# Performance work log

Hardware: AMD Instinct MI355X
Metric: run time of the kernel (lower is better)

## Reference

```python
import jax, jax.numpy as jnp
import numpy as np
from math import sqrt

DIM = 256
HEADS = 4
GROUPS = min(DIM // 4, 32)  # = 32
EPS = 1e-6


def setup_inputs() -> dict:
    key = jax.random.key(0)
    ks = jax.random.split(key, 10)
    B, C, H, W = 16, DIM, 32, 32
    x = jax.random.normal(ks[0], (B, C, H, W), dtype=jnp.float32)
    s = 1.0 / sqrt(C)
    inp = {
        'x': x,
        'gn_scale': jnp.ones((C,), jnp.float32),
        'gn_bias': jnp.zeros((C,), jnp.float32),
        'Wq': jax.random.normal(ks[1], (C, C), jnp.float32) * s,
        'bq': jnp.zeros((C,), jnp.float32),
        'Wk': jax.random.normal(ks[2], (C, C), jnp.float32) * s,
        'bk': jnp.zeros((C,), jnp.float32),
        'Wv': jax.random.normal(ks[3], (C, C), jnp.float32) * s,
        'bv': jnp.zeros((C,), jnp.float32),
        'Wp': jax.random.normal(ks[4], (C, C), jnp.float32) * s,
        'bp': jnp.zeros((C,), jnp.float32),
    }
    return inp


def _group_norm(x, scale, bias):
    B, C, H, W = x.shape
    xg = x.reshape(B, GROUPS, C // GROUPS, H, W)
    mean = xg.mean(axis=(2, 3, 4), keepdims=True)
    var = xg.var(axis=(2, 3, 4), keepdims=True)
    xg = (xg - mean) * jax.lax.rsqrt(var + EPS)
    x = xg.reshape(B, C, H, W)
    return x * scale[None, :, None, None] + bias[None, :, None, None]


def _lin_ch(x, W, b):
    # 1x1 conv / linear over channel dim: (B,C,H,W) x (C,Cout) -> (B,Cout,H,W)
    return jnp.einsum('bchw,cd->bdhw', x, W) + b[None, :, None, None]


def reference(x, gn_scale, gn_bias, Wq, bq, Wk, bk, Wv, bv, Wp, bp):
    B, C, H, W = x.shape
    dh = C // HEADS
    _x = _group_norm(x, gn_scale, gn_bias)
    q = _lin_ch(_x, Wq, bq).reshape(B, HEADS, dh, H, W)
    k = _lin_ch(_x, Wk, bk).reshape(B, HEADS, dh, H, W)
    v = _lin_ch(_x, Wv, bv).reshape(B, HEADS, dh, H, W)
    scores = jnp.einsum('bhdxy,bhdij->bhxyij', q, k) / sqrt(C)
    scores = scores.reshape(B, HEADS, H, W, H * W)
    weights = jax.nn.softmax(scores, axis=-1).reshape(B, HEADS, H, W, H, W)
    h = jnp.einsum('bhxyij,bhdij->bhdxy', weights, v).reshape(B, C, H, W)
    h = _lin_ch(h, Wp, bp)
    ret = (x + h) / sqrt(2.0)
    return ret
```

## Files before the change

kernel.cpp:

```cpp
#include <hip/hip_runtime.h>
#include <hip/hip_bf16.h>

#define BATCH 16
#define CH    256
#define HW    1024
#define NH    4
#define DH    64
#define NG    32
#define CPG   8
#define EPSV  1e-6f

#define QSCALE 0.090168440055558706f

typedef __bf16 bf16x8 __attribute__((ext_vector_type(8)));
typedef float  f32x4  __attribute__((ext_vector_type(4)));

__device__ __forceinline__ unsigned short f2bf(float f) {
    union { __hip_bfloat16 h; unsigned short u; } cv;
    cv.h = __float2bfloat16(f);
    return cv.u;
}

__device__ __forceinline__ unsigned int fbits(float f) {
    union { float f; unsigned int u; } cv; cv.f = f; return cv.u;
}

__device__ __forceinline__ void gld_lds16(const unsigned short* g, unsigned short* l) {
    __builtin_amdgcn_global_load_lds(
        (const __attribute__((address_space(1))) void*)g,
        (__attribute__((address_space(3))) void*)l, 16, 0, 0);
}

__global__ void prep_kernel(const float* Wq, const float* Wk, const float* Wv,
                            const float* Wp, const float* bq, const float* bk,
                            const float* bv, unsigned short* wqkv_t,
                            unsigned short* wp_t, float* bqkv) {
    int idx = blockIdx.x * 256 + threadIdx.x;
    if (idx < 768 * 256) {
        int n = idx >> 8, c = idx & 255;
        const float* W = (n < 256) ? Wq : (n < 512) ? Wk : Wv;
        int d = n & 255;
        wqkv_t[idx] = f2bf(W[c * 256 + d]);
    } else if (idx < 768 * 256 + 256 * 256) {
        int j = idx - 768 * 256;
        int n = j >> 8, c = j & 255;
        wp_t[j] = f2bf(Wp[c * 256 + n]);
    }
    if (idx < 768)
        bqkv[idx] = (idx < 256) ? bq[idx] : (idx < 512) ? bk[idx - 256] : bv[idx - 512];
}

__global__ void gn_stats_kernel(const float* x, const float* scale, const float* bias,
                                float* coefA, float* coefB) {
    int bg = blockIdx.x;
    const float4* p = reinterpret_cast<const float4*>(x + (size_t)bg * (CPG * HW));
    int t = threadIdx.x;
    float s = 0.f, ss = 0.f;
    for (int i = t; i < CPG * HW / 4; i += 256) {
        float4 v = p[i];
        s += v.x + v.y + v.z + v.w;
        ss += v.x * v.x + v.y * v.y + v.z * v.z + v.w * v.w;
    }
    for (int o = 32; o; o >>= 1) { s += __shfl_down(s, o); ss += __shfl_down(ss, o); }
    __shared__ float as[4], ass[4];
    int w = t >> 6;
    if ((t & 63) == 0) { as[w] = s; ass[w] = ss; }
    __syncthreads();
    if (t < 8) {
        float S = as[0] + as[1] + as[2] + as[3];
        float SS = ass[0] + ass[1] + ass[2] + ass[3];
        float mean = S / (float)(CPG * HW);
        float var = SS / (float)(CPG * HW) - mean * mean;
        float rstd = rsqrtf(var + EPSV);
        int b = bg >> 5, g = bg & 31;
        int c = g * CPG + t;
        float a = rstd * scale[c];
        coefA[b * CH + c] = a;
        coefB[b * CH + c] = bias[c] - mean * a;
    }
}

__global__ __launch_bounds__(256) void qkv_kernel(const float* x,
        const float* coefA, const float* coefB,
        const unsigned short* wqkv_t, const float* bqkv,
        unsigned short* qb, unsigned short* kb, unsigned short* vb) {
    int t = threadIdx.x;
    int wv = t >> 6, lane = t & 63, quad = lane >> 4, ln = lane & 15;
    int wr = wv >> 1, wc = wv & 1;
    int bx = blockIdx.x;
    int m0 = bx * 128 + wr * 64;
    int n0 = blockIdx.y * 128 + wc * 64;
    int bb = bx >> 3;
    int p0 = (bx & 7) * 128;

    __shared__ __align__(16) unsigned short lds_a[128][40];

    const float* xb = x + (size_t)bb * CH * HW + p0;
    const float* cA = coefA + bb * CH;
    const float* cB = coefB + bb * CH;

    int sp = t & 127;
    int sbase = (t >> 7) * 2;

    f32x4 acc[4][4] = {};
    for (int k0 = 0; k0 < CH; k0 += 32) {
        bf16x8 wpk[2];
#pragma unroll
        for (int rep = 0; rep < 2; rep++) {
            int s = sbase + rep;
            int cb = k0 + s * 8;
            union { bf16x8 v8; __hip_bfloat162 h2[4]; } u;
#pragma unroll
            for (int j = 0; j < 4; j++) {
                float v0 = fmaf(xb[(size_t)(cb + 2 * j)     * HW + sp], cA[cb + 2 * j],     cB[cb + 2 * j]);
                float v1 = fmaf(xb[(size_t)(cb + 2 * j + 1) * HW + sp], cA[cb + 2 * j + 1], cB[cb + 2 * j + 1]);
                u.h2[j] = __float22bfloat162_rn(float2{v0, v1});
            }
            wpk[rep] = u.v8;
        }
        __syncthreads();
#pragma unroll
        for (int rep = 0; rep < 2; rep++) {
            int s = sbase + rep;
            int phys = s ^ (sp & 3);
            *reinterpret_cast<bf16x8*>(&lds_a[sp][phys * 8]) = wpk[rep];
        }
        __syncthreads();
        bf16x8 af[4], bfr[4];
#pragma unroll
        for (int i = 0; i < 4; i++) {
            int p = wr * 64 + i * 16 + ln;
            af[i] = *reinterpret_cast<const bf16x8*>(&lds_a[p][(quad ^ (p & 3)) * 8]);
        }
#pragma unroll
        for (int j = 0; j < 4; j++)
            bfr[j] = *reinterpret_cast<const bf16x8*>(
                wqkv_t + (size_t)(n0 + j * 16 + ln) * CH + k0 + quad * 8);
#pragma unroll
        for (int i = 0; i < 4; i++)
#pragma unroll
            for (int j = 0; j < 4; j++)
                acc[i][j] = __builtin_amdgcn_mfma_f32_16x16x32_bf16(af[i], bfr[j], acc[i][j], 0, 0, 0);
    }
#pragma unroll
    for (int j = 0; j < 4; j++) {
        int n = n0 + j * 16 + ln;
        float bias = bqkv[n];
        int which = n >> 8;
        int dh_ = n & 255;
        int head = dh_ >> 6, d = dh_ & 63;
#pragma unroll
        for (int i = 0; i < 4; i++) {
            int mb = m0 + i * 16 + quad * 4;
            int bi = mb >> 10, p = mb & 1023;
            int bh = bi * NH + head;
            if (which < 2) {
                unsigned short* dst = (which == 0 ? qb : kb) + (size_t)bh * HW * DH;
                float sc = (which == 0) ? QSCALE : 1.0f;
#pragma unroll
                for (int r = 0; r < 4; r++)
                    dst[(size_t)(p + r) * DH + d] = f2bf((acc[i][j][r] + bias) * sc);
            } else {
                unsigned short* dst = vb + ((size_t)bh * DH + d) * HW + p;
                ushort4 pk4;
                pk4.x = f2bf(acc[i][j][0] + bias);
                pk4.y = f2bf(acc[i][j][1] + bias);
                pk4.z = f2bf(acc[i][j][2] + bias);
                pk4.w = f2bf(acc[i][j][3] + bias);
                *reinterpret_cast<ushort4*>(dst) = pk4;
            }
        }
    }
}

__global__ __launch_bounds__(256) void attn_kernel(const unsigned short* qb,
        const unsigned short* kb, const unsigned short* vb, unsigned short* h_t) {
    int qblk = blockIdx.x, bh = blockIdx.y;
    int t = threadIdx.x;
    int wv = t >> 6, lane = t & 63, quad = lane >> 4, ln = lane & 15;
    int q0 = qblk * 128 + wv * 32;

    const unsigned short* Q = qb + (size_t)bh * HW * DH;
    const unsigned short* K = kb + (size_t)bh * HW * DH;
    const unsigned short* V = vb + (size_t)bh * DH * HW;

    __shared__ __align__(16) unsigned short kbuf[2][4096];
    __shared__ __align__(16) unsigned short vbuf[2][4096];
    __shared__ __align__(16) unsigned short pbuf[4][2][16][72];

    int c_a = wv * 64 + lane;
    int c_b = 256 + wv * 64 + lane;
    int pa = c_a >> 3, ja = (c_a & 7) ^ (pa & 7);
    int pb = c_b >> 3, jb = (c_b & 7) ^ (pb & 7);
    const unsigned short* pka = K + (size_t)pa * DH + ja * 8;
    const unsigned short* pkb = K + (size_t)pb * DH + jb * 8;
    const unsigned short* pva = V + (size_t)pa * HW + ja * 8;
    const unsigned short* pvb = V + (size_t)pb * HW + jb * 8;
    int lofs_a = wv * 512, lofs_b = 2048 + wv * 512;

    int koffs[4][2];
#pragma unroll
    for (int mt = 0; mt < 4; mt++) {
        int p = mt * 16 + ln, sw = p & 7;
#pragma unroll
        for (int kk = 0; kk < 2; kk++)
            koffs[mt][kk] = p * 64 + (((kk * 4 + quad) ^ sw) * 8);
    }

    bf16x8 qf[2][2];
#pragma unroll
    for (int nq = 0; nq < 2; nq++)
#pragma unroll
        for (int kk = 0; kk < 2; kk++)
            qf[nq][kk] = *reinterpret_cast<const bf16x8*>(
                Q + (size_t)(q0 + nq * 16 + ln) * DH + kk * 32 + quad * 8);

    f32x4 ls[2] = {};
    f32x4 o[2][4] = {};

    gld_lds16(pka, &kbuf[0][lofs_a]);
    gld_lds16(pkb, &kbuf[0][lofs_b]);
    gld_lds16(pva, &vbuf[0][lofs_a]);
    gld_lds16(pvb, &vbuf[0][lofs_b]);
    pka += 64 * DH; pkb += 64 * DH; pva += 64; pvb += 64;

#define ATTN_TILE(B, DO_STAGE)                                                      \
    {                                                                               \
        __syncthreads();                                                            \
        if (DO_STAGE) {                                                             \
            gld_lds16(pka, &kbuf[B ^ 1][lofs_a]);                                   \
            gld_lds16(pkb, &kbuf[B ^ 1][lofs_b]);                                   \
            gld_lds16(pva, &vbuf[B ^ 1][lofs_a]);                                   \
            gld_lds16(pvb, &vbuf[B ^ 1][lofs_b]);                                   \
            pka += 64 * DH; pkb += 64 * DH; pva += 64; pvb += 64;                   \
        }                                                                           \
        bf16x8 kf[4][2], vf[4][2];                                                  \
        _Pragma("unroll")                                                           \
        for (int mt = 0; mt < 4; mt++) {                                            \
            _Pragma("unroll")                                                       \
            for (int kk = 0; kk < 2; kk++) {                                        \
                kf[mt][kk] = *reinterpret_cast<const bf16x8*>(&kbuf[B][koffs[mt][kk]]); \
                vf[mt][kk] = *reinterpret_cast<const bf16x8*>(&vbuf[B][koffs[mt][kk]]); \
            }                                                                       \
        }                                                                           \
        f32x4 s[2][4] = {};                                                         \
        _Pragma("unroll")                                                           \
        for (int nq = 0; nq < 2; nq++)                                              \
            _Pragma("unroll")                                                       \
            for (int mt = 0; mt < 4; mt++) {                                        \
                s[nq][mt] = __builtin_amdgcn_mfma_f32_16x16x32_bf16(kf[mt][0], qf[nq][0], s[nq][mt], 0, 0, 0); \
                s[nq][mt] = __builtin_amdgcn_mfma_f32_16x16x32_bf16(kf[mt][1], qf[nq][1], s[nq][mt], 0, 0, 0); \
            }                                                                       \
        _Pragma("unroll")                                                           \
        for (int nq = 0; nq < 2; nq++)                                              \
            _Pragma("unroll")                                                       \
            for (int mt = 0; mt < 4; mt++) {                                        \
                float e0 = __builtin_amdgcn_exp2f(s[nq][mt][0]);                    \
                float e1 = __builtin_amdgcn_exp2f(s[nq][mt][1]);                    \
                float e2 = __builtin_amdgcn_exp2f(s[nq][mt][2]);                    \
                float e3 = __builtin_amdgcn_exp2f(s[nq][mt][3]);                    \
                ls[nq][0] += e0; ls[nq][1] += e1;                                   \
                ls[nq][2] += e2; ls[nq][3] += e3;                                   \
                uint2 pk2;                                                          \
                pk2.x = __builtin_amdgcn_perm(fbits(e1), fbits(e0), 0x07060302u);   \
                pk2.y = __builtin_amdgcn_perm(fbits(e3), fbits(e2), 0x07060302u);   \
                *reinterpret_cast<uint2*>(&pbuf[wv][nq][ln][mt * 16 + quad * 4]) = pk2; \
            }                                                                       \
        _Pragma("unroll")                                                           \
        for (int nq = 0; nq < 2; nq++)                                              \
            _Pragma("unroll")                                                       \
            for (int kk = 0; kk < 2; kk++) {                                        \
                bf16x8 pf = *reinterpret_cast<const bf16x8*>(&pbuf[wv][nq][ln][kk * 32 + quad * 8]); \
                _Pragma("unroll")                                                   \
                for (int mt = 0; mt < 4; mt++)                                      \
                    o[nq][mt] = __builtin_amdgcn_mfma_f32_16x16x32_bf16(vf[mt][kk], pf, o[nq][mt], 0, 0, 0); \
            }                                                                       \
    }

    for (int u = 0; u < 8; u++) {
        ATTN_TILE(0, true)
        ATTN_TILE(1, (u < 7))
    }
#undef ATTN_TILE

    int b_ = bh >> 2, head = bh & 3;
#pragma unroll
    for (int nq = 0; nq < 2; nq++) {
        float lsum = ls[nq][0] + ls[nq][1] + ls[nq][2] + ls[nq][3];
        lsum += __shfl_xor(lsum, 16);
        lsum += __shfl_xor(lsum, 32);
        float inv = 1.0f / lsum;
        unsigned short* dst = h_t + ((size_t)b_ * HW + q0 + nq * 16 + ln) * CH + head * DH;
#pragma unroll
        for (int mt = 0; mt < 4; mt++) {
            ushort4 pk4;
            pk4.x = f2bf(o[nq][mt][0] * inv);
            pk4.y = f2bf(o[nq][mt][1] * inv);
            pk4.z = f2bf(o[nq][mt][2] * inv);
            pk4.w = f2bf(o[nq][mt][3] * inv);
            *reinterpret_cast<ushort4*>(dst + mt * 16 + quad * 4) = pk4;
        }
    }
}

__global__ __launch_bounds__(256) void proj_kernel(const unsigned short* h_t,
        const unsigned short* wp_t, const float* bp, const float* x, float* out) {
    int t = threadIdx.x;
    int wv = t >> 6, lane = t & 63, quad = lane >> 4, ln = lane & 15;
    int wr = wv >> 1, wc = wv & 1;
    int m0 = blockIdx.x * 64 + wr * 32;
    int n0 = blockIdx.y * 128 + wc * 64;

    f32x4 acc[2][4] = {};
    for (int k0 = 0; k0 < CH; k0 += 32) {
        int koff = k0 + quad * 8;
        bf16x8 af[2], bfr[4];
#pragma unroll
        for (int i = 0; i < 2; i++)
            af[i] = *reinterpret_cast<const bf16x8*>(h_t + (size_t)(m0 + i * 16 + ln) * CH + koff);
#pragma unroll
        for (int j = 0; j < 4; j++)
            bfr[j] = *reinterpret_cast<const bf16x8*>(wp_t + (size_t)(n0 + j * 16 + ln) * CH + koff);
#pragma unroll
        for (int i = 0; i < 2; i++)
#pragma unroll
            for (int j = 0; j < 4; j++)
                acc[i][j] = __builtin_amdgcn_mfma_f32_16x16x32_bf16(af[i], bfr[j], acc[i][j], 0, 0, 0);
    }
    const float inv_s2 = 0.70710678118654752440f;
#pragma unroll
    for (int j = 0; j < 4; j++) {
        int n = n0 + j * 16 + ln;
        float bias = bp[n];
#pragma unroll
        for (int i = 0; i < 2; i++) {
            int mb = m0 + i * 16 + quad * 4;
            int bi = mb >> 10, p = mb & 1023;
            size_t off = ((size_t)(bi * CH + n)) * HW + p;
            float4 xv = *reinterpret_cast<const float4*>(x + off);
            float4 ov;
            ov.x = (xv.x + acc[i][j][0] + bias) * inv_s2;
            ov.y = (xv.y + acc[i][j][1] + bias) * inv_s2;
            ov.z = (xv.z + acc[i][j][2] + bias) * inv_s2;
            ov.w = (xv.w + acc[i][j][3] + bias) * inv_s2;
            *reinterpret_cast<float4*>(out + off) = ov;
        }
    }
}

extern "C" void kernel_launch(void* const* d_in, const int* in_sizes, int n_in,
                              void* d_out, int out_size, void* d_ws, size_t ws_size,
                              hipStream_t stream) {
    const float* x        = (const float*)d_in[0];
    const float* gn_scale = (const float*)d_in[1];
    const float* gn_bias  = (const float*)d_in[2];
    const float* Wq = (const float*)d_in[3];
    const float* bq = (const float*)d_in[4];
    const float* Wk = (const float*)d_in[5];
    const float* bk = (const float*)d_in[6];
    const float* Wv = (const float*)d_in[7];
    const float* bv = (const float*)d_in[8];
    const float* Wp = (const float*)d_in[9];
    const float* bp = (const float*)d_in[10];
    float* out = (float*)d_out;

    char* ws = (char*)d_ws;
    float*          bqkv   = (float*)(ws + 0);
    float*          coefA  = (float*)(ws + 4096);
    float*          coefB  = (float*)(ws + 20480);
    unsigned short* wqkv_t = (unsigned short*)(ws + 36864);
    unsigned short* wp_t   = (unsigned short*)(ws + 430080);
    unsigned short* h_t    = (unsigned short*)(ws + 1048576);
    unsigned short* qb     = (unsigned short*)(ws + 9437184);
    unsigned short* kb     = (unsigned short*)(ws + 17825792);
    unsigned short* vb     = (unsigned short*)(ws + 26214400);

    prep_kernel<<<1024, 256, 0, stream>>>(Wq, Wk, Wv, Wp, bq, bk, bv, wqkv_t, wp_t, bqkv);
    gn_stats_kernel<<<512, 256, 0, stream>>>(x, gn_scale, gn_bias, coefA, coefB);
    qkv_kernel<<<dim3(128, 6), 256, 0, stream>>>(x, coefA, coefB, wqkv_t, bqkv, qb, kb, vb);
    attn_kernel<<<dim3(8, 64), 256, 0, stream>>>(qb, kb, vb, h_t);
    proj_kernel<<<dim3(256, 2), 256, 0, stream>>>(h_t, wp_t, bp, x, out);
}
```

Measured before the change: 162.3 us.

## Split attention over two key halves, add combine kernel, merge prep kernels

The attention kernel now splits the 1024 keys into two slices along a third grid dimension. Each slice writes an unnormalized bf16 partial output plus its row sums, and a new combine kernel adds the two and normalizes. This doubles the number of attention blocks so the GPU is better filled. The weight-prep and GroupNorm-stats kernels are merged into one launch, and the projection GEMM is retiled to 16-row blocks with four waves covering all 256 output columns. In exchange there is extra global traffic for the partial buffers, an added launch, and bf16 rounding of the partial sums before normalization.

```diff
diff --git a/kernel.cpp b/kernel.cpp
--- a/kernel.cpp
+++ b/kernel.cpp
@@ -25,36 +25,41 @@
     union { float f; unsigned int u; } cv; cv.f = f; return cv.u;
 }
 
+__device__ __forceinline__ float bfu(unsigned int u) {
+    union { unsigned int u; float f; } cv; cv.u = u; return cv.f;
+}
+
 __device__ __forceinline__ void gld_lds16(const unsigned short* g, unsigned short* l) {
     __builtin_amdgcn_global_load_lds(
         (const __attribute__((address_space(1))) void*)g,
         (__attribute__((address_space(3))) void*)l, 16, 0, 0);
 }
 
-__global__ void prep_kernel(const float* Wq, const float* Wk, const float* Wv,
-                            const float* Wp, const float* bq, const float* bk,
-                            const float* bv, unsigned short* wqkv_t,
-                            unsigned short* wp_t, float* bqkv) {
-    int idx = blockIdx.x * 256 + threadIdx.x;
-    if (idx < 768 * 256) {
-        int n = idx >> 8, c = idx & 255;
-        const float* W = (n < 256) ? Wq : (n < 512) ? Wk : Wv;
-        int d = n & 255;
-        wqkv_t[idx] = f2bf(W[c * 256 + d]);
-    } else if (idx < 768 * 256 + 256 * 256) {
-        int j = idx - 768 * 256;
-        int n = j >> 8, c = j & 255;
-        wp_t[j] = f2bf(Wp[c * 256 + n]);
-    }
-    if (idx < 768)
-        bqkv[idx] = (idx < 256) ? bq[idx] : (idx < 512) ? bk[idx - 256] : bv[idx - 512];
-}
-
-__global__ void gn_stats_kernel(const float* x, const float* scale, const float* bias,
-                                float* coefA, float* coefB) {
+__global__ void prep_stats_kernel(const float* x, const float* scale, const float* bias,
+                                  const float* Wq, const float* Wk, const float* Wv,
+                                  const float* Wp, const float* bq, const float* bk,
+                                  const float* bv, float* coefA, float* coefB,
+                                  unsigned short* wqkv_t, unsigned short* wp_t,
+                                  float* bqkv) {
+    int t = threadIdx.x;
+    if (blockIdx.x >= 512) {
+        int idx = (blockIdx.x - 512) * 256 + t;
+        if (idx < 768 * 256) {
+            int n = idx >> 8, c = idx & 255;
+            const float* W = (n < 256) ? Wq : (n < 512) ? Wk : Wv;
+            int d = n & 255;
+            wqkv_t[idx] = f2bf(W[c * 256 + d]);
+        } else if (idx < 768 * 256 + 256 * 256) {
+            int j = idx - 768 * 256;
+            int n = j >> 8, c = j & 255;
+            wp_t[j] = f2bf(Wp[c * 256 + n]);
+        }
+        if (idx < 768)
+            bqkv[idx] = (idx < 256) ? bq[idx] : (idx < 512) ? bk[idx - 256] : bv[idx - 512];
+        return;
+    }
     int bg = blockIdx.x;
     const float4* p = reinterpret_cast<const float4*>(x + (size_t)bg * (CPG * HW));
-    int t = threadIdx.x;
     float s = 0.f, ss = 0.f;
     for (int i = t; i < CPG * HW / 4; i += 256) {
         float4 v = p[i];
@@ -174,15 +179,17 @@
 }
 
 __global__ __launch_bounds__(256) void attn_kernel(const unsigned short* qb,
-        const unsigned short* kb, const unsigned short* vb, unsigned short* h_t) {
-    int qblk = blockIdx.x, bh = blockIdx.y;
+        const unsigned short* kb, const unsigned short* vb,
+        unsigned short* opart0, unsigned short* opart1,
+        float* lsum0, float* lsum1) {
+    int qblk = blockIdx.x, bh = blockIdx.y, ksl = blockIdx.z;
     int t = threadIdx.x;
     int wv = t >> 6, lane = t & 63, quad = lane >> 4, ln = lane & 15;
     int q0 = qblk * 128 + wv * 32;
 
     const unsigned short* Q = qb + (size_t)bh * HW * DH;
-    const unsigned short* K = kb + (size_t)bh * HW * DH;
-    const unsigned short* V = vb + (size_t)bh * DH * HW;
+    const unsigned short* K = kb + (size_t)bh * HW * DH + (size_t)ksl * 512 * DH;
+    const unsigned short* V = vb + (size_t)bh * DH * HW + ksl * 512;
 
     __shared__ __align__(16) unsigned short kbuf[2][4096];
     __shared__ __align__(16) unsigned short vbuf[2][4096];
@@ -277,74 +284,93 @@
             }                                                                       \
     }
 
-    for (int u = 0; u < 8; u++) {
+    for (int u = 0; u < 4; u++) {
         ATTN_TILE(0, true)
-        ATTN_TILE(1, (u < 7))
+        ATTN_TILE(1, (u < 3))
     }
 #undef ATTN_TILE
 
+    unsigned short* opart = ksl ? opart1 : opart0;
+    float* lsum = ksl ? lsum1 : lsum0;
     int b_ = bh >> 2, head = bh & 3;
 #pragma unroll
     for (int nq = 0; nq < 2; nq++) {
-        float lsum = ls[nq][0] + ls[nq][1] + ls[nq][2] + ls[nq][3];
-        lsum += __shfl_xor(lsum, 16);
-        lsum += __shfl_xor(lsum, 32);
-        float inv = 1.0f / lsum;
-        unsigned short* dst = h_t + ((size_t)b_ * HW + q0 + nq * 16 + ln) * CH + head * DH;
+        float lv = ls[nq][0] + ls[nq][1] + ls[nq][2] + ls[nq][3];
+        lv += __shfl_xor(lv, 16);
+        lv += __shfl_xor(lv, 32);
+        int q = q0 + nq * 16 + ln;
+        if (lane < 16)
+            lsum[((b_ * HW + q) << 2) + head] = lv;
+        unsigned short* dst = opart + ((size_t)(b_ * HW + q)) * CH + head * DH;
 #pragma unroll
         for (int mt = 0; mt < 4; mt++) {
             ushort4 pk4;
-            pk4.x = f2bf(o[nq][mt][0] * inv);
-            pk4.y = f2bf(o[nq][mt][1] * inv);
-            pk4.z = f2bf(o[nq][mt][2] * inv);
-            pk4.w = f2bf(o[nq][mt][3] * inv);
+            pk4.x = f2bf(o[nq][mt][0]);
+            pk4.y = f2bf(o[nq][mt][1]);
+            pk4.z = f2bf(o[nq][mt][2]);
+            pk4.w = f2bf(o[nq][mt][3]);
             *reinterpret_cast<ushort4*>(dst + mt * 16 + quad * 4) = pk4;
         }
     }
+}
+
+__global__ __launch_bounds__(256) void combine_kernel(const unsigned short* o1,
+        const unsigned short* o2, const float* l1, const float* l2,
+        unsigned short* h_t) {
+    int tid = blockIdx.x * 256 + threadIdx.x;
+    int base = tid * 8;
+    int lidx = ((base >> 8) << 2) + ((base >> 6) & 3);
+    float inv = 1.0f / (l1[lidx] + l2[lidx]);
+    uint4 a = *reinterpret_cast<const uint4*>(o1 + base);
+    uint4 b = *reinterpret_cast<const uint4*>(o2 + base);
+    unsigned int av[4] = {a.x, a.y, a.z, a.w};
+    unsigned int bv4[4] = {b.x, b.y, b.z, b.w};
+    unsigned int rv[4];
+#pragma unroll
+    for (int i = 0; i < 4; i++) {
+        float g0 = (bfu(av[i] << 16) + bfu(bv4[i] << 16)) * inv;
+        float g1 = (bfu(av[i] & 0xffff0000u) + bfu(bv4[i] & 0xffff0000u)) * inv;
+        union { __hip_bfloat162 h2; unsigned int u; } cv;
+        cv.h2 = __float22bfloat162_rn(float2{g0, g1});
+        rv[i] = cv.u;
+    }
+    *reinterpret_cast<uint4*>(h_t + base) = make_uint4(rv[0], rv[1], rv[2], rv[3]);
 }
 
 __global__ __launch_bounds__(256) void proj_kernel(const unsigned short* h_t,
         const unsigned short* wp_t, const float* bp, const float* x, float* out) {
     int t = threadIdx.x;
     int wv = t >> 6, lane = t & 63, quad = lane >> 4, ln = lane & 15;
-    int wr = wv >> 1, wc = wv & 1;
-    int m0 = blockIdx.x * 64 + wr * 32;
-    int n0 = blockIdx.y * 128 + wc * 64;
-
-    f32x4 acc[2][4] = {};
+    int m0 = blockIdx.x * 16;
+    int n0 = wv * 64;
+
+    f32x4 acc[4] = {};
     for (int k0 = 0; k0 < CH; k0 += 32) {
         int koff = k0 + quad * 8;
-        bf16x8 af[2], bfr[4];
-#pragma unroll
-        for (int i = 0; i < 2; i++)
-            af[i] = *reinterpret_cast<const bf16x8*>(h_t + (size_t)(m0 + i * 16 + ln) * CH + koff);
+        bf16x8 af = *reinterpret_cast<const bf16x8*>(h_t + (size_t)(m0 + ln) * CH + koff);
+        bf16x8 bfr[4];
 #pragma unroll
         for (int j = 0; j < 4; j++)
             bfr[j] = *reinterpret_cast<const bf16x8*>(wp_t + (size_t)(n0 + j * 16 + ln) * CH + koff);
 #pragma unroll
-        for (int i = 0; i < 2; i++)
-#pragma unroll
-            for (int j = 0; j < 4; j++)
-                acc[i][j] = __builtin_amdgcn_mfma_f32_16x16x32_bf16(af[i], bfr[j], acc[i][j], 0, 0, 0);
+        for (int j = 0; j < 4; j++)
+            acc[j] = __builtin_amdgcn_mfma_f32_16x16x32_bf16(af, bfr[j], acc[j], 0, 0, 0);
     }
     const float inv_s2 = 0.70710678118654752440f;
+    int mb = m0 + quad * 4;
+    int bi = mb >> 10, p = mb & 1023;
 #pragma unroll
     for (int j = 0; j < 4; j++) {
         int n = n0 + j * 16 + ln;
         float bias = bp[n];
-#pragma unroll
-        for (int i = 0; i < 2; i++) {
-            int mb = m0 + i * 16 + quad * 4;
-            int bi = mb >> 10, p = mb & 1023;
-            size_t off = ((size_t)(bi * CH + n)) * HW + p;
-            float4 xv = *reinterpret_cast<const float4*>(x + off);
-            float4 ov;
-            ov.x = (xv.x + acc[i][j][0] + bias) * inv_s2;
-            ov.y = (xv.y + acc[i][j][1] + bias) * inv_s2;
-            ov.z = (xv.z + acc[i][j][2] + bias) * inv_s2;
-            ov.w = (xv.w + acc[i][j][3] + bias) * inv_s2;
-            *reinterpret_cast<float4*>(out + off) = ov;
-        }
+        size_t off = ((size_t)(bi * CH + n)) * HW + p;
+        float4 xv = *reinterpret_cast<const float4*>(x + off);
+        float4 ov;
+        ov.x = (xv.x + acc[j][0] + bias) * inv_s2;
+        ov.y = (xv.y + acc[j][1] + bias) * inv_s2;
+        ov.z = (xv.z + acc[j][2] + bias) * inv_s2;
+        ov.w = (xv.w + acc[j][3] + bias) * inv_s2;
+        *reinterpret_cast<float4*>(out + off) = ov;
     }
 }
 
@@ -374,10 +400,15 @@
     unsigned short* qb     = (unsigned short*)(ws + 9437184);
     unsigned short* kb     = (unsigned short*)(ws + 17825792);
     unsigned short* vb     = (unsigned short*)(ws + 26214400);
-
-    prep_kernel<<<1024, 256, 0, stream>>>(Wq, Wk, Wv, Wp, bq, bk, bv, wqkv_t, wp_t, bqkv);
-    gn_stats_kernel<<<512, 256, 0, stream>>>(x, gn_scale, gn_bias, coefA, coefB);
+    unsigned short* opart0 = (unsigned short*)(ws + 34603008);
+    unsigned short* opart1 = (unsigned short*)(ws + 42991616);
+    float*          lsum0  = (float*)(ws + 51380224);
+    float*          lsum1  = (float*)(ws + 51642368);
+
+    prep_stats_kernel<<<1536, 256, 0, stream>>>(x, gn_scale, gn_bias, Wq, Wk, Wv, Wp,
+                                                bq, bk, bv, coefA, coefB, wqkv_t, wp_t, bqkv);
     qkv_kernel<<<dim3(128, 6), 256, 0, stream>>>(x, coefA, coefB, wqkv_t, bqkv, qb, kb, vb);
-    attn_kernel<<<dim3(8, 64), 256, 0, stream>>>(qb, kb, vb, h_t);
-    proj_kernel<<<dim3(256, 2), 256, 0, stream>>>(h_t, wp_t, bp, x, out);
-}
+    attn_kernel<<<dim3(8, 64, 2), 256, 0, stream>>>(qb, kb, vb, opart0, opart1, lsum0, lsum1);
+    combine_kernel<<<4096, 256, 0, stream>>>(opart0, opart1, lsum0, lsum1, h_t);
+    proj_kernel<<<dim3(1024, 1), 256, 0, stream>>>(h_t, wp_t, bp, x, out);
+}
```

Measured after the change: 178.0 us. 1.1x slower.
